# Kernel tuning notes

Measured on AMD Instinct MI355X. Metric: run time of the kernel, lower is better.

## Reference

```python
import jax, jax.numpy as jnp
from jax import lax
import numpy as np

BINS = 256

def setup_inputs() -> dict:
    key = jax.random.key(0)
    k1, k2 = jax.random.split(key)
    B, C, H, W = 8, 3, 1024, 1024
    dst = jax.random.uniform(k1, (B, C, H, W), dtype=jnp.float32)
    ref = jax.random.uniform(k2, (B, C, H, W), dtype=jnp.float32)
    return {"dst": dst, "ref": ref}


def _cal_hist(img):
    # img: [B,C,H,W] in [0,1]. torch.histc(img*255, bins=256, min=0, max=255):
    # bin width = 255/256, so bin = floor(img*255 / (255/256)) = floor(img*256).
    # Inputs are in [0,1) so nothing is out of histc's range (clip is a no-op safeguard).
    B, C, H, W = img.shape
    bc = B * C
    x = img.reshape(bc, H * W)
    idx = jnp.clip(jnp.floor(x * float(BINS)).astype(jnp.int32), 0, BINS - 1)
    rows = jnp.arange(bc, dtype=jnp.int32)[:, None]
    counts = jnp.zeros((bc, BINS), jnp.float32).at[rows, idx].add(1.0)
    # F.normalize(p=1, dim=1) with eps=1e-12
    counts = counts / jnp.maximum(jnp.sum(counts, axis=1, keepdims=True), 1e-12)
    # triu-bmm == cumulative sum -> per-channel CDF
    return jnp.cumsum(counts, axis=1)


def _trans_row(cdf_dst, cdf_ref):
    # Faithful vectorization of the sequential two-pointer loop in cal_trans.
    # For each i (pointer j only ever advances): match at the smallest
    # j' >= j with cdf_ref[j'-1] <= d <= cdf_ref[j']; if impossible, j runs
    # off to 256 and this and all later entries become 255.
    def step(j, d):
        s = jnp.searchsorted(cdf_ref, d)            # smallest s with cdf_ref[s] >= d, in [0,256]
        cand = jnp.maximum(j, s)                    # pointer never moves backwards; cand in [1,256]
        ok = (j < BINS) & (cand <= BINS - 1) & (d >= cdf_ref[cand - 1])
        out = jnp.where(ok, cand, BINS - 1)
        j_next = jnp.where(ok, cand, jnp.int32(BINS))
        return j_next, out.astype(jnp.int32)
    _, tail = lax.scan(step, jnp.int32(1), cdf_dst[1:])  # i = 1..255
    table = jnp.concatenate([jnp.zeros(1, jnp.int32), tail])  # table[0] = arange init = 0
    return table.at[BINS - 1].set(BINS - 1)                   # table[:,255] = 255


def reference(dst, ref):
    B, C, H, W = dst.shape
    bc = B * C
    hist_dst = _cal_hist(dst)   # [BC,256] CDFs
    hist_ref = _cal_hist(ref)
    tables = jax.vmap(_trans_row)(hist_dst, hist_ref)  # [BC,256] int32
    # NOTE: original code indexes tables[b*c] (not b*C+c) -- bug preserved faithfully.
    b_idx = jnp.arange(B, dtype=jnp.int32)[:, None]
    c_idx = jnp.arange(C, dtype=jnp.int32)[None, :]
    row_sel = (b_idx * c_idx).reshape(-1)               # [BC]
    luts = tables[row_sel]                              # [BC,256]
    pix = jnp.clip((dst * 255.0).astype(jnp.int32), 0, BINS - 1).reshape(bc, H * W)
    rst = jnp.take_along_axis(luts, pix, axis=1).reshape(B, C, H, W)
    return rst.astype(dst.dtype) / 255.0
```

## Files before the change

kernel.cpp:

```cpp
#include <hip/hip_runtime.h>

#define BINS 256
#define BC_N 24
#define C_N  3
#define NROWS 12
#define CH   85
#define ACH  128

__global__ __launch_bounds__(256) void hm_hist(const float* __restrict__ dst,
                                               const float* __restrict__ refp,
                                               unsigned int* __restrict__ part,
                                               int n4_per_row) {
    __shared__ unsigned int shist[BINS];
    __shared__ unsigned int wsum[BINS];

    const int t = threadIdx.x;
    const int l = t & 63;
    const int w = t >> 6;

    shist[t] = 0u;
    __syncthreads();

    const int y = blockIdx.y;
    const int row = (y < 9) ? y : 2 * y - 8;
    const float* img = blockIdx.z ? refp : dst;
    const float4* p = reinterpret_cast<const float4*>(img) + (size_t)row * n4_per_row;

    const int span = (n4_per_row + CH - 1) / CH;
    const int lo = blockIdx.x * span;
    const int hi = min(lo + span, n4_per_row);
    const int n  = hi - lo;
    const int SB = ((n * 19) / 100) & ~63;
    const int mid = hi - SB;

    if (w < 3) {
        for (int i = lo + w * 64 + l; i < mid; i += 192) {
            float4 v = p[i];
            atomicAdd(&shist[min((int)(v.x * 256.0f), 255)], 1u);
            atomicAdd(&shist[min((int)(v.y * 256.0f), 255)], 1u);
            atomicAdd(&shist[min((int)(v.z * 256.0f), 255)], 1u);
            atomicAdd(&shist[min((int)(v.w * 256.0f), 255)], 1u);
        }
    } else {
        const unsigned long long t0 = (l & 1)  ? 0ull : ~0ull;
        const unsigned long long t1 = (l & 2)  ? 0ull : ~0ull;
        const unsigned long long t2 = (l & 4)  ? 0ull : ~0ull;
        const unsigned long long t3 = (l & 8)  ? 0ull : ~0ull;
        const unsigned long long t4 = (l & 16) ? 0ull : ~0ull;
        const unsigned long long t5 = (l & 32) ? 0ull : ~0ull;
        unsigned int c0 = 0, c1 = 0, c2 = 0, c3 = 0;

        auto grp = [&](float x) {
            int bin = min((int)(x * 256.0f), 255);
            unsigned long long B0 = __ballot(bin & 1);
            unsigned long long B1 = __ballot(bin & 2);
            unsigned long long B2 = __ballot(bin & 4);
            unsigned long long B3 = __ballot(bin & 8);
            unsigned long long B4 = __ballot(bin & 16);
            unsigned long long B5 = __ballot(bin & 32);
            unsigned long long B6 = __ballot(bin & 64);
            unsigned long long B7 = __ballot(bin & 128);
            unsigned long long m = (B0 ^ t0) & (B1 ^ t1) & (B2 ^ t2)
                                 & (B3 ^ t3) & (B4 ^ t4) & (B5 ^ t5);
            unsigned long long a = m & ~B7, b = m & B7;
            c0 += (unsigned)__popcll(a & ~B6);
            c1 += (unsigned)__popcll(a &  B6);
            c2 += (unsigned)__popcll(b & ~B6);
            c3 += (unsigned)__popcll(b &  B6);
        };

        const int nk = SB >> 6;
        if (nk > 0) {
            float4 v = p[mid + l];
            for (int k = 0; k + 1 < nk; ++k) {
                float4 nv = p[mid + ((k + 1) << 6) + l];
                __builtin_amdgcn_sched_barrier(0);
                grp(v.x); grp(v.y); grp(v.z); grp(v.w);
                v = nv;
            }
            grp(v.x); grp(v.y); grp(v.z); grp(v.w);
        }
        wsum[l]       = c0;
        wsum[l + 64]  = c1;
        wsum[l + 128] = c2;
        wsum[l + 192] = c3;
    }
    __syncthreads();

    part[(((size_t)blockIdx.z * NROWS + y) * CH + blockIdx.x) * BINS + t]
        = shist[t] + wsum[t];
}

__global__ __launch_bounds__(256) void hm_table(const unsigned int* __restrict__ part,
                                                float* __restrict__ lut) {
    __shared__ unsigned int sd[BINS], sr[BINS];
    __shared__ float cdf_d[BINS], cdf_r[BINS];
    __shared__ int firstFail;

    const int r = blockIdx.x;
    const int t = threadIdx.x;

    const unsigned int* pd = part + ((size_t)0 * NROWS + r) * CH * BINS;
    const unsigned int* pr = part + ((size_t)1 * NROWS + r) * CH * BINS;
    unsigned int xd = 0, xr = 0;
    #pragma unroll 5
    for (int k = 0; k < CH; ++k) {
        xd += pd[k * BINS + t];
        xr += pr[k * BINS + t];
    }
    if (t == 0) firstFail = BINS;
    sd[t] = xd; sr[t] = xr;
    __syncthreads();

    #pragma unroll
    for (int off = 1; off < BINS; off <<= 1) {
        unsigned int yd = (t >= off) ? sd[t - off] : 0u;
        unsigned int yr = (t >= off) ? sr[t - off] : 0u;
        __syncthreads();
        xd += yd; xr += yr;
        sd[t] = xd; sr[t] = xr;
        __syncthreads();
    }
    float totd = fmaxf((float)sd[BINS - 1], 1e-12f);
    float totr = fmaxf((float)sr[BINS - 1], 1e-12f);
    cdf_d[t] = (float)xd / totd;
    cdf_r[t] = (float)xr / totr;
    __syncthreads();

    int out;
    if (t == 0) {
        out = 0;
    } else {
        float d = cdf_d[t];
        int lo = 0, hi = BINS;
        while (lo < hi) {
            int m = (lo + hi) >> 1;
            if (cdf_r[m] < d) lo = m + 1; else hi = m;
        }
        int cand = lo > 1 ? lo : 1;
        bool ok = (cand <= BINS - 1) && (d >= cdf_r[cand - 1]);
        if (!ok) atomicMin(&firstFail, t);
        out = cand;
    }
    __syncthreads();

    if (t >= firstFail) out = BINS - 1;
    if (t == BINS - 1) out = BINS - 1;
    lut[(size_t)r * BINS + t] = (float)out / 255.0f;
}

__global__ __launch_bounds__(256) void hm_apply(const float* __restrict__ dst,
                                                const float* __restrict__ lut,
                                                float* __restrict__ out,
                                                int n4_per_row) {
    __shared__ float slut[BINS];
    const int bc = blockIdx.y;
    const int b = bc / C_N;
    const int c = bc - b * C_N;
    const int r = b * c;
    const int cr = (r <= 8) ? r : 8 + ((r - 8) >> 1);
    const int t = threadIdx.x;

    slut[t] = lut[(size_t)cr * BINS + t];
    __syncthreads();

    const float4* in4 = reinterpret_cast<const float4*>(dst) + (size_t)bc * n4_per_row;
    float4* out4 = reinterpret_cast<float4*>(out) + (size_t)bc * n4_per_row;
    const int gsz = gridDim.x * 256;

    int i = blockIdx.x * 256 + t;
    for (; i + gsz < n4_per_row; i += 2 * gsz) {
        float4 v0 = in4[i];
        float4 v1 = in4[i + gsz];
        __builtin_amdgcn_sched_barrier(0);
        float4 o0, o1;
        o0.x = slut[min(max((int)(v0.x * 255.0f), 0), 255)];
        o0.y = slut[min(max((int)(v0.y * 255.0f), 0), 255)];
        o0.z = slut[min(max((int)(v0.z * 255.0f), 0), 255)];
        o0.w = slut[min(max((int)(v0.w * 255.0f), 0), 255)];
        o1.x = slut[min(max((int)(v1.x * 255.0f), 0), 255)];
        o1.y = slut[min(max((int)(v1.y * 255.0f), 0), 255)];
        o1.z = slut[min(max((int)(v1.z * 255.0f), 0), 255)];
        o1.w = slut[min(max((int)(v1.w * 255.0f), 0), 255)];
        out4[i] = o0;
        out4[i + gsz] = o1;
    }
    for (; i < n4_per_row; i += gsz) {
        float4 v = in4[i];
        float4 o;
        o.x = slut[min(max((int)(v.x * 255.0f), 0), 255)];
        o.y = slut[min(max((int)(v.y * 255.0f), 0), 255)];
        o.z = slut[min(max((int)(v.z * 255.0f), 0), 255)];
        o.w = slut[min(max((int)(v.w * 255.0f), 0), 255)];
        out4[i] = o;
    }
}

extern "C" void kernel_launch(void* const* d_in, const int* in_sizes, int n_in,
                              void* d_out, int out_size, void* d_ws, size_t ws_size,
                              hipStream_t stream) {
    const float* dst  = (const float*)d_in[0];
    const float* refp = (const float*)d_in[1];
    float* out = (float*)d_out;

    const int total = in_sizes[0];
    const int hw = total / BC_N;
    const int n4 = hw >> 2;

    unsigned int* part = (unsigned int*)d_ws;
    float* lut = (float*)((char*)d_ws + (size_t)2 * NROWS * CH * BINS * sizeof(unsigned int));

    dim3 hg(CH, NROWS, 2);
    hm_hist<<<hg, dim3(256), 0, stream>>>(dst, refp, part, n4);

    hm_table<<<dim3(NROWS), dim3(256), 0, stream>>>(part, lut);

    dim3 ag(ACH, BC_N);
    hm_apply<<<ag, dim3(256), 0, stream>>>(dst, lut, out, n4);
}
```

Measured before the change: 66.81 us.

## Rebalance histogram waves: one atomic wave, three ballot-based counting waves

Reassigns the four waves in the histogram kernel. One wave now handles the shared-memory atomic path, with three float4 loads batched per iteration. The other three waves run the ballot/popcount counting path over interleaved 64-element groups, and the split fraction rises from about 19% to 41%. Per-wave ballot results go into separate shared arrays that are summed at the end. The aim is to reduce LDS atomic contention and balance the two paths, at the cost of more ALU work on the ballot side and a possible load imbalance between waves.

```diff
diff --git a/kernel.cpp b/kernel.cpp
--- a/kernel.cpp
+++ b/kernel.cpp
@@ -12,7 +12,7 @@
                                                unsigned int* __restrict__ part,
                                                int n4_per_row) {
     __shared__ unsigned int shist[BINS];
-    __shared__ unsigned int wsum[BINS];
+    __shared__ unsigned int wsum[3][BINS];
 
     const int t = threadIdx.x;
     const int l = t & 63;
@@ -30,11 +30,30 @@
     const int lo = blockIdx.x * span;
     const int hi = min(lo + span, n4_per_row);
     const int n  = hi - lo;
-    const int SB = ((n * 19) / 100) & ~63;
+    const int SB = ((n * 41) / 100) & ~63;
     const int mid = hi - SB;
 
-    if (w < 3) {
-        for (int i = lo + w * 64 + l; i < mid; i += 192) {
+    if (w == 0) {
+        int base = lo;
+        for (; base + 192 <= mid; base += 192) {
+            float4 v0 = p[base + l];
+            float4 v1 = p[base + 64 + l];
+            float4 v2 = p[base + 128 + l];
+            __builtin_amdgcn_sched_barrier(0);
+            atomicAdd(&shist[min((int)(v0.x * 256.0f), 255)], 1u);
+            atomicAdd(&shist[min((int)(v0.y * 256.0f), 255)], 1u);
+            atomicAdd(&shist[min((int)(v0.z * 256.0f), 255)], 1u);
+            atomicAdd(&shist[min((int)(v0.w * 256.0f), 255)], 1u);
+            atomicAdd(&shist[min((int)(v1.x * 256.0f), 255)], 1u);
+            atomicAdd(&shist[min((int)(v1.y * 256.0f), 255)], 1u);
+            atomicAdd(&shist[min((int)(v1.z * 256.0f), 255)], 1u);
+            atomicAdd(&shist[min((int)(v1.w * 256.0f), 255)], 1u);
+            atomicAdd(&shist[min((int)(v2.x * 256.0f), 255)], 1u);
+            atomicAdd(&shist[min((int)(v2.y * 256.0f), 255)], 1u);
+            atomicAdd(&shist[min((int)(v2.z * 256.0f), 255)], 1u);
+            atomicAdd(&shist[min((int)(v2.w * 256.0f), 255)], 1u);
+        }
+        for (int i = base + l; i < mid; i += 64) {
             float4 v = p[i];
             atomicAdd(&shist[min((int)(v.x * 256.0f), 255)], 1u);
             atomicAdd(&shist[min((int)(v.y * 256.0f), 255)], 1u);
@@ -69,26 +88,27 @@
             c3 += (unsigned)__popcll(b &  B6);
         };
 
-        const int nk = SB >> 6;
-        if (nk > 0) {
-            float4 v = p[mid + l];
-            for (int k = 0; k + 1 < nk; ++k) {
-                float4 nv = p[mid + ((k + 1) << 6) + l];
+        const int ng = SB >> 6;
+        int g = w - 1;
+        if (g < ng) {
+            float4 v = p[mid + (g << 6) + l];
+            for (; g + 3 < ng; g += 3) {
+                float4 nv = p[mid + ((g + 3) << 6) + l];
                 __builtin_amdgcn_sched_barrier(0);
                 grp(v.x); grp(v.y); grp(v.z); grp(v.w);
                 v = nv;
             }
             grp(v.x); grp(v.y); grp(v.z); grp(v.w);
         }
-        wsum[l]       = c0;
-        wsum[l + 64]  = c1;
-        wsum[l + 128] = c2;
-        wsum[l + 192] = c3;
+        wsum[w - 1][l]       = c0;
+        wsum[w - 1][l + 64]  = c1;
+        wsum[w - 1][l + 128] = c2;
+        wsum[w - 1][l + 192] = c3;
     }
     __syncthreads();
 
     part[(((size_t)blockIdx.z * NROWS + y) * CH + blockIdx.x) * BINS + t]
-        = shist[t] + wsum[t];
+        = shist[t] + wsum[0][t] + wsum[1][t] + wsum[2][t];
 }
 
 __global__ __launch_bounds__(256) void hm_table(const unsigned int* __restrict__ part,
```

Result: slower. 70.20 us (+5.1%).
